# Kernel optimization log

Measured on AMD Instinct MI355X. Metric: run time of the kernel, lower is better.

Reference implementation:

```python
import jax, jax.numpy as jnp
import numpy as np

N_NODES = 2_000_000
N_EDGES = 16_777_216
N_REL = 4


def setup_inputs() -> dict:
    key = jax.random.key(0)
    ks = jax.random.split(key, 13)
    inp = {
        "author_x": jax.random.normal(ks[0], (N_NODES, 4), jnp.float32),
        "paper_x": jax.random.normal(ks[1], (N_NODES, 4), jnp.float32),
        "src_index": jax.random.randint(ks[2], (N_EDGES,), 0, N_NODES, jnp.int64 if jax.config.jax_enable_x64 else jnp.int32).astype(jnp.int32),
        "dst_index": jax.random.randint(ks[3], (N_EDGES,), 0, N_NODES).astype(jnp.int32),
        "edge_type_index": jax.random.randint(ks[4], (N_EDGES,), 0, N_REL).astype(jnp.int32),
        "edge_src_is_paper": jax.random.randint(ks[5], (N_REL,), 0, 2).astype(jnp.int32),
        "edge_dst_is_paper": jax.random.randint(ks[6], (N_REL,), 0, 2).astype(jnp.int32),
        "Wa": jax.random.normal(ks[7], (4, 4), jnp.float32) * 0.5,
        "ba": jax.random.normal(ks[8], (4,), jnp.float32) * 0.1,
        "Wp": jax.random.normal(ks[9], (4, 4), jnp.float32) * 0.5,
        "bp": jax.random.normal(ks[10], (4,), jnp.float32) * 0.1,
        "Ws": jax.random.normal(ks[11], (8,), jnp.float32) * 0.5,
        "bs": jax.random.normal(ks[12], (1,), jnp.float32) * 0.1,
    }
    return inp


def reference(author_x, paper_x, src_index, dst_index, edge_type_index,
              edge_src_is_paper, edge_dst_is_paper, Wa, ba, Wp, bp, Ws, bs):
    # Encode node tables (tiny GEMMs): [N,4] @ [4,4]^T + [4]
    author_h = author_x @ Wa.T + ba
    paper_h = paper_x @ Wp.T + bp
    # Per-edge relation-type dispatch: 1 = paper table, 0 = author table
    src_p = edge_src_is_paper[edge_type_index].astype(bool)  # [E]
    dst_p = edge_dst_is_paper[edge_type_index].astype(bool)  # [E]
    src_repr = jnp.where(src_p[:, None], paper_h[src_index], author_h[src_index])  # [E,4]
    dst_repr = jnp.where(dst_p[:, None], paper_h[dst_index], author_h[dst_index])  # [E,4]
    # scorer: Linear(8,1) on concat, squeeze last dim -> [E]
    logits = jnp.concatenate([src_repr, dst_repr], axis=-1) @ Ws + bs[0]
    return logits
```

## Files before the change

kernel.cpp:

```cpp
#include <hip/hip_runtime.h>

typedef int         iv4 __attribute__((ext_vector_type(4)));
typedef float       fv4 __attribute__((ext_vector_type(4)));
typedef _Float16    hv4 __attribute__((ext_vector_type(4)));
typedef signed char cv4 __attribute__((ext_vector_type(4)));

struct Fold {
    float va_s[4], va_d[4], vp_s[4], vp_d[4];
    float ca_s, ca_d, cp_s, cp_d;
};

__device__ inline Fold make_fold(const float* __restrict__ Wa, const float* __restrict__ ba,
                                 const float* __restrict__ Wp, const float* __restrict__ bp,
                                 const float* __restrict__ Ws) {
    Fold f;
    float w0 = Ws[0], w1 = Ws[1], w2 = Ws[2], w3 = Ws[3];
    float w4 = Ws[4], w5 = Ws[5], w6 = Ws[6], w7 = Ws[7];
#pragma unroll
    for (int j = 0; j < 4; ++j) {
        f.va_s[j] = w0*Wa[j] + w1*Wa[4+j] + w2*Wa[8+j] + w3*Wa[12+j];
        f.va_d[j] = w4*Wa[j] + w5*Wa[4+j] + w6*Wa[8+j] + w7*Wa[12+j];
        f.vp_s[j] = w0*Wp[j] + w1*Wp[4+j] + w2*Wp[8+j] + w3*Wp[12+j];
        f.vp_d[j] = w4*Wp[j] + w5*Wp[4+j] + w6*Wp[8+j] + w7*Wp[12+j];
    }
    f.ca_s = w0*ba[0] + w1*ba[1] + w2*ba[2] + w3*ba[3];
    f.ca_d = w4*ba[0] + w5*ba[1] + w6*ba[2] + w7*ba[3];
    f.cp_s = w0*bp[0] + w1*bp[1] + w2*bp[2] + w3*bp[3];
    f.cp_d = w4*bp[0] + w5*bp[1] + w6*bp[2] + w7*bp[3];
    return f;
}

__device__ inline void node_scores(const Fold& f, fv4 a, fv4 p,
                                   float& as, float& ps, float& ad, float& pd) {
    as = a.x*f.va_s[0] + a.y*f.va_s[1] + a.z*f.va_s[2] + a.w*f.va_s[3] + f.ca_s;
    ad = a.x*f.va_d[0] + a.y*f.va_d[1] + a.z*f.va_d[2] + a.w*f.va_d[3] + f.ca_d;
    ps = p.x*f.vp_s[0] + p.y*f.vp_s[1] + p.z*f.vp_s[2] + p.w*f.vp_s[3] + f.cp_s;
    pd = p.x*f.vp_d[0] + p.y*f.vp_d[1] + p.z*f.vp_d[2] + p.w*f.vp_d[3] + f.cp_d;
}

__global__ __launch_bounds__(256) void node_pass1(
    const fv4* __restrict__ ax, const fv4* __restrict__ px,
    const float* __restrict__ Wa, const float* __restrict__ ba,
    const float* __restrict__ Wp, const float* __restrict__ bp,
    const float* __restrict__ Ws,
    hv4* __restrict__ sc, unsigned* __restrict__ maxes, int n)
{
    Fold f = make_fold(Wa, ba, Wp, bp, Ws);
    float ms = 0.f, md = 0.f;
    int stride = gridDim.x * blockDim.x;
    for (int i = blockIdx.x * blockDim.x + threadIdx.x; i < n; i += stride) {
        fv4 a = __builtin_nontemporal_load(ax + i);
        fv4 p = __builtin_nontemporal_load(px + i);
        float as, ps, ad, pd;
        node_scores(f, a, p, as, ps, ad, pd);
        hv4 h;
        h.x = (_Float16)as; h.y = (_Float16)ps; h.z = (_Float16)ad; h.w = (_Float16)pd;
        __builtin_nontemporal_store(h, sc + i);
        ms = fmaxf(ms, fmaxf(fabsf(as), fabsf(ps)));
        md = fmaxf(md, fmaxf(fabsf(ad), fabsf(pd)));
    }
#pragma unroll
    for (int off = 32; off >= 1; off >>= 1) {
        ms = fmaxf(ms, __shfl_down(ms, off));
        md = fmaxf(md, __shfl_down(md, off));
    }
    __shared__ float lms[4], lmd[4];
    int wave = threadIdx.x >> 6, lane = threadIdx.x & 63;
    if (lane == 0) { lms[wave] = ms; lmd[wave] = md; }
    __syncthreads();
    if (threadIdx.x == 0) {
        float bms = fmaxf(fmaxf(lms[0], lms[1]), fmaxf(lms[2], lms[3]));
        float bmd = fmaxf(fmaxf(lmd[0], lmd[1]), fmaxf(lmd[2], lmd[3]));
        atomicMax(&maxes[0], __float_as_uint(bms));
        atomicMax(&maxes[1], __float_as_uint(bmd));
    }
}

__global__ __launch_bounds__(256) void node_pass2(
    const hv4* __restrict__ sc, const unsigned* __restrict__ maxes,
    signed char* __restrict__ ts, signed char* __restrict__ td, int n)
{
    int i = blockIdx.x * blockDim.x + threadIdx.x;
    if (i >= n) return;
    float inv_s = 127.f / fmaxf(__uint_as_float(maxes[0]), 1e-20f);
    float inv_d = 127.f / fmaxf(__uint_as_float(maxes[1]), 1e-20f);
    hv4 h = __builtin_nontemporal_load(sc + i);
    int qas = min(127, max(-127, __float2int_rn((float)h.x * inv_s)));
    int qps = min(127, max(-127, __float2int_rn((float)h.y * inv_s)));
    int qad = min(127, max(-127, __float2int_rn((float)h.z * inv_d)));
    int qpd = min(127, max(-127, __float2int_rn((float)h.w * inv_d)));
    cv4 dummy;
    (void)dummy;
    ((short*)ts)[i] = (short)(((qps & 0xff) << 8) | (qas & 0xff));
    ((short*)td)[i] = (short)(((qpd & 0xff) << 8) | (qad & 0xff));
}

__global__ __launch_bounds__(256) void edge_src_pass(
    const iv4* __restrict__ src, const iv4* __restrict__ et,
    const int* __restrict__ esp,
    const signed char* __restrict__ ts, cv4* __restrict__ qsrc, int n4)
{
    int i = blockIdx.x * blockDim.x + threadIdx.x;
    if (i >= n4) return;
    unsigned smask = (unsigned)((esp[0]&1) | ((esp[1]&1)<<1) | ((esp[2]&1)<<2) | ((esp[3]&1)<<3));
    iv4 s = __builtin_nontemporal_load(src + i);
    iv4 t = __builtin_nontemporal_load(et  + i);
    cv4 q;
    q.x = ts[2*s.x + (int)((smask >> t.x) & 1u)];
    q.y = ts[2*s.y + (int)((smask >> t.y) & 1u)];
    q.z = ts[2*s.z + (int)((smask >> t.z) & 1u)];
    q.w = ts[2*s.w + (int)((smask >> t.w) & 1u)];
    __builtin_nontemporal_store(q, qsrc + i);
}

__global__ __launch_bounds__(256) void edge_dst_pass(
    const iv4* __restrict__ dst, const iv4* __restrict__ et,
    const int* __restrict__ edp, const float* __restrict__ bs,
    const unsigned* __restrict__ maxes,
    const signed char* __restrict__ td, const cv4* __restrict__ qsrc,
    fv4* __restrict__ out, int n4)
{
    int i = blockIdx.x * blockDim.x + threadIdx.x;
    if (i >= n4) return;
    unsigned dmask = (unsigned)((edp[0]&1) | ((edp[1]&1)<<1) | ((edp[2]&1)<<2) | ((edp[3]&1)<<3));
    float b = bs[0];
    float scale_s = __uint_as_float(maxes[0]) * (1.f / 127.f);
    float scale_d = __uint_as_float(maxes[1]) * (1.f / 127.f);

    iv4 d = __builtin_nontemporal_load(dst + i);
    iv4 t = __builtin_nontemporal_load(et  + i);
    cv4 qs = __builtin_nontemporal_load(qsrc + i);
    signed char q0 = td[2*d.x + (int)((dmask >> t.x) & 1u)];
    signed char q1 = td[2*d.y + (int)((dmask >> t.y) & 1u)];
    signed char q2 = td[2*d.z + (int)((dmask >> t.z) & 1u)];
    signed char q3 = td[2*d.w + (int)((dmask >> t.w) & 1u)];

    fv4 o;
    o.x = (float)qs.x * scale_s + (float)q0 * scale_d + b;
    o.y = (float)qs.y * scale_s + (float)q1 * scale_d + b;
    o.z = (float)qs.z * scale_s + (float)q2 * scale_d + b;
    o.w = (float)qs.w * scale_s + (float)q3 * scale_d + b;
    __builtin_nontemporal_store(o, out + i);
}

__global__ __launch_bounds__(256) void fused_kernel(
    const fv4* __restrict__ ax, const fv4* __restrict__ px,
    const int* __restrict__ src, const int* __restrict__ dst, const int* __restrict__ et,
    const int* __restrict__ esp, const int* __restrict__ edp,
    const float* __restrict__ Wa, const float* __restrict__ ba,
    const float* __restrict__ Wp, const float* __restrict__ bp,
    const float* __restrict__ Ws, const float* __restrict__ bs,
    float* __restrict__ out, int n)
{
    int e = blockIdx.x * blockDim.x + threadIdx.x;
    if (e >= n) return;
    Fold f = make_fold(Wa, ba, Wp, bp, Ws);
    int t = et[e];
    int sp = esp[t] & 1, dp = edp[t] & 1;
    fv4 sv = sp ? px[src[e]] : ax[src[e]];
    fv4 dv = dp ? px[dst[e]] : ax[dst[e]];
    float ssc = sp ? (sv.x*f.vp_s[0] + sv.y*f.vp_s[1] + sv.z*f.vp_s[2] + sv.w*f.vp_s[3] + f.cp_s)
                   : (sv.x*f.va_s[0] + sv.y*f.va_s[1] + sv.z*f.va_s[2] + sv.w*f.va_s[3] + f.ca_s);
    float dsc = dp ? (dv.x*f.vp_d[0] + dv.y*f.vp_d[1] + dv.z*f.vp_d[2] + dv.w*f.vp_d[3] + f.cp_d)
                   : (dv.x*f.va_d[0] + dv.y*f.va_d[1] + dv.z*f.va_d[2] + dv.w*f.va_d[3] + f.ca_d);
    out[e] = ssc + dsc + bs[0];
}

extern "C" void kernel_launch(void* const* d_in, const int* in_sizes, int n_in,
                              void* d_out, int out_size, void* d_ws, size_t ws_size,
                              hipStream_t stream) {
    const float* ax  = (const float*)d_in[0];
    const float* px  = (const float*)d_in[1];
    const int*   src = (const int*)d_in[2];
    const int*   dst = (const int*)d_in[3];
    const int*   et  = (const int*)d_in[4];
    const int*   esp = (const int*)d_in[5];
    const int*   edp = (const int*)d_in[6];
    const float* Wa  = (const float*)d_in[7];
    const float* ba  = (const float*)d_in[8];
    const float* Wp  = (const float*)d_in[9];
    const float* bp  = (const float*)d_in[10];
    const float* Ws  = (const float*)d_in[11];
    const float* bs  = (const float*)d_in[12];
    float* out = (float*)d_out;

    const int n_nodes = in_sizes[0] / 4;
    const int n_edges = in_sizes[2];

    size_t union_sz = (size_t)n_edges > (size_t)n_nodes * 8 ? (size_t)n_edges : (size_t)n_nodes * 8;
    union_sz = (union_sz + 255) & ~(size_t)255;
    const size_t off_u  = 256;
    const size_t off_ts = off_u + union_sz;
    const size_t off_td = off_ts + (size_t)n_nodes * 2;
    const size_t need   = off_td + (size_t)n_nodes * 2;

    if (ws_size >= need && (n_edges & 3) == 0) {
        unsigned* maxes = (unsigned*)d_ws;
        hv4* sc   = (hv4*)((char*)d_ws + off_u);
        cv4* qsrc = (cv4*)((char*)d_ws + off_u);
        signed char* ts = (signed char*)((char*)d_ws + off_ts);
        signed char* td = (signed char*)((char*)d_ws + off_td);

        (void)hipMemsetAsync(maxes, 0, 2 * sizeof(unsigned), stream);
        node_pass1<<<512, 256, 0, stream>>>(
            (const fv4*)ax, (const fv4*)px, Wa, ba, Wp, bp, Ws, sc, maxes, n_nodes);
        node_pass2<<<(n_nodes + 255) / 256, 256, 0, stream>>>(
            sc, maxes, ts, td, n_nodes);

        const int n4 = n_edges / 4;
        const int nb = (n4 + 255) / 256;
        edge_src_pass<<<nb, 256, 0, stream>>>(
            (const iv4*)src, (const iv4*)et, esp, ts, qsrc, n4);
        edge_dst_pass<<<nb, 256, 0, stream>>>(
            (const iv4*)dst, (const iv4*)et, edp, bs, maxes,
            td, (const cv4*)qsrc, (fv4*)out, n4);
    } else {
        fused_kernel<<<(n_edges + 255) / 256, 256, 0, stream>>>(
            (const fv4*)ax, (const fv4*)px, src, dst, et, esp, edp,
            Wa, ba, Wp, bp, Ws, bs, out, n_edges);
    }
}
```

Measured before the change: 432.1 us.

## Pack dst-side relation bit into src intermediate to skip edge_type reread

The src edge pass now writes a 16-bit value per edge: the quantized src score plus the dst-is-paper bit derived from the edge type. The dst pass reads this instead of rereading the edge_type array, which removes one full streaming pass over the edge types. Each thread also processes 16 edges instead of 4. The cost is a larger intermediate buffer (2 bytes per edge instead of 1) and a bigger workspace requirement, with a fallback to the old path if that requirement is not met.

Result: slower. 459.1 us (+6.3%).

```diff
diff --git a/kernel.cpp b/kernel.cpp
--- a/kernel.cpp
+++ b/kernel.cpp
@@ -4,6 +4,7 @@
 typedef float       fv4 __attribute__((ext_vector_type(4)));
 typedef _Float16    hv4 __attribute__((ext_vector_type(4)));
 typedef signed char cv4 __attribute__((ext_vector_type(4)));
+typedef short       sv8 __attribute__((ext_vector_type(8)));
 
 struct Fold {
     float va_s[4], va_d[4], vp_s[4], vp_d[4];
@@ -89,10 +90,88 @@
     int qps = min(127, max(-127, __float2int_rn((float)h.y * inv_s)));
     int qad = min(127, max(-127, __float2int_rn((float)h.z * inv_d)));
     int qpd = min(127, max(-127, __float2int_rn((float)h.w * inv_d)));
-    cv4 dummy;
-    (void)dummy;
     ((short*)ts)[i] = (short)(((qps & 0xff) << 8) | (qas & 0xff));
     ((short*)td)[i] = (short)(((qpd & 0xff) << 8) | (qad & 0xff));
+}
+
+__device__ inline void gather4(const signed char* __restrict__ ts,
+                               unsigned smask, unsigned dmask,
+                               iv4 s, iv4 t, short* r) {
+    r[0] = (short)((unsigned char)ts[2*s.x + (int)((smask >> t.x) & 1u)] | ((int)((dmask >> t.x) & 1u) << 8));
+    r[1] = (short)((unsigned char)ts[2*s.y + (int)((smask >> t.y) & 1u)] | ((int)((dmask >> t.y) & 1u) << 8));
+    r[2] = (short)((unsigned char)ts[2*s.z + (int)((smask >> t.z) & 1u)] | ((int)((dmask >> t.z) & 1u) << 8));
+    r[3] = (short)((unsigned char)ts[2*s.w + (int)((smask >> t.w) & 1u)] | ((int)((dmask >> t.w) & 1u) << 8));
+}
+
+__global__ __launch_bounds__(256) void edge_src_pass16(
+    const iv4* __restrict__ src, const iv4* __restrict__ et,
+    const int* __restrict__ esp, const int* __restrict__ edp,
+    const signed char* __restrict__ ts, sv8* __restrict__ qs, int n16)
+{
+    int i = blockIdx.x * blockDim.x + threadIdx.x;
+    if (i >= n16) return;
+    unsigned smask = (unsigned)((esp[0]&1) | ((esp[1]&1)<<1) | ((esp[2]&1)<<2) | ((esp[3]&1)<<3));
+    unsigned dmask = (unsigned)((edp[0]&1) | ((edp[1]&1)<<1) | ((edp[2]&1)<<2) | ((edp[3]&1)<<3));
+    int base = i * 4;
+    iv4 s0 = __builtin_nontemporal_load(src + base);
+    iv4 s1 = __builtin_nontemporal_load(src + base + 1);
+    iv4 s2 = __builtin_nontemporal_load(src + base + 2);
+    iv4 s3 = __builtin_nontemporal_load(src + base + 3);
+    iv4 t0 = __builtin_nontemporal_load(et + base);
+    iv4 t1 = __builtin_nontemporal_load(et + base + 1);
+    iv4 t2 = __builtin_nontemporal_load(et + base + 2);
+    iv4 t3 = __builtin_nontemporal_load(et + base + 3);
+    short r[16];
+    gather4(ts, smask, dmask, s0, t0, r + 0);
+    gather4(ts, smask, dmask, s1, t1, r + 4);
+    gather4(ts, smask, dmask, s2, t2, r + 8);
+    gather4(ts, smask, dmask, s3, t3, r + 12);
+    sv8 a, b;
+#pragma unroll
+    for (int k = 0; k < 8; ++k) { a[k] = r[k]; b[k] = r[8 + k]; }
+    __builtin_nontemporal_store(a, qs + 2*i);
+    __builtin_nontemporal_store(b, qs + 2*i + 1);
+}
+
+__device__ inline fv4 combine4(const signed char* __restrict__ td, iv4 d,
+                               const short* r, float scale_s, float scale_d, float b) {
+    fv4 o;
+    o.x = (float)(signed char)(r[0] & 0xff) * scale_s + (float)td[2*d.x + ((r[0] >> 8) & 1)] * scale_d + b;
+    o.y = (float)(signed char)(r[1] & 0xff) * scale_s + (float)td[2*d.y + ((r[1] >> 8) & 1)] * scale_d + b;
+    o.z = (float)(signed char)(r[2] & 0xff) * scale_s + (float)td[2*d.z + ((r[2] >> 8) & 1)] * scale_d + b;
+    o.w = (float)(signed char)(r[3] & 0xff) * scale_s + (float)td[2*d.w + ((r[3] >> 8) & 1)] * scale_d + b;
+    return o;
+}
+
+__global__ __launch_bounds__(256) void edge_dst_pass16(
+    const iv4* __restrict__ dst, const float* __restrict__ bs,
+    const unsigned* __restrict__ maxes,
+    const signed char* __restrict__ td, const sv8* __restrict__ qs,
+    fv4* __restrict__ out, int n16)
+{
+    int i = blockIdx.x * blockDim.x + threadIdx.x;
+    if (i >= n16) return;
+    float b = bs[0];
+    float scale_s = __uint_as_float(maxes[0]) * (1.f / 127.f);
+    float scale_d = __uint_as_float(maxes[1]) * (1.f / 127.f);
+    int base = i * 4;
+    iv4 d0 = __builtin_nontemporal_load(dst + base);
+    iv4 d1 = __builtin_nontemporal_load(dst + base + 1);
+    iv4 d2 = __builtin_nontemporal_load(dst + base + 2);
+    iv4 d3 = __builtin_nontemporal_load(dst + base + 3);
+    sv8 qa = __builtin_nontemporal_load(qs + 2*i);
+    sv8 qb = __builtin_nontemporal_load(qs + 2*i + 1);
+    short r[16];
+#pragma unroll
+    for (int k = 0; k < 8; ++k) { r[k] = qa[k]; r[8 + k] = qb[k]; }
+    fv4 o0 = combine4(td, d0, r + 0,  scale_s, scale_d, b);
+    fv4 o1 = combine4(td, d1, r + 4,  scale_s, scale_d, b);
+    fv4 o2 = combine4(td, d2, r + 8,  scale_s, scale_d, b);
+    fv4 o3 = combine4(td, d3, r + 12, scale_s, scale_d, b);
+    __builtin_nontemporal_store(o0, out + base);
+    __builtin_nontemporal_store(o1, out + base + 1);
+    __builtin_nontemporal_store(o2, out + base + 2);
+    __builtin_nontemporal_store(o3, out + base + 3);
 }
 
 __global__ __launch_bounds__(256) void edge_src_pass(
@@ -126,20 +205,14 @@
     float b = bs[0];
     float scale_s = __uint_as_float(maxes[0]) * (1.f / 127.f);
     float scale_d = __uint_as_float(maxes[1]) * (1.f / 127.f);
-
     iv4 d = __builtin_nontemporal_load(dst + i);
     iv4 t = __builtin_nontemporal_load(et  + i);
-    cv4 qs = __builtin_nontemporal_load(qsrc + i);
-    signed char q0 = td[2*d.x + (int)((dmask >> t.x) & 1u)];
-    signed char q1 = td[2*d.y + (int)((dmask >> t.y) & 1u)];
-    signed char q2 = td[2*d.z + (int)((dmask >> t.z) & 1u)];
-    signed char q3 = td[2*d.w + (int)((dmask >> t.w) & 1u)];
-
+    cv4 qsv = __builtin_nontemporal_load(qsrc + i);
     fv4 o;
-    o.x = (float)qs.x * scale_s + (float)q0 * scale_d + b;
-    o.y = (float)qs.y * scale_s + (float)q1 * scale_d + b;
-    o.z = (float)qs.z * scale_s + (float)q2 * scale_d + b;
-    o.w = (float)qs.w * scale_s + (float)q3 * scale_d + b;
+    o.x = (float)qsv.x * scale_s + (float)td[2*d.x + (int)((dmask >> t.x) & 1u)] * scale_d + b;
+    o.y = (float)qsv.y * scale_s + (float)td[2*d.y + (int)((dmask >> t.y) & 1u)] * scale_d + b;
+    o.z = (float)qsv.z * scale_s + (float)td[2*d.z + (int)((dmask >> t.z) & 1u)] * scale_d + b;
+    o.w = (float)qsv.w * scale_s + (float)td[2*d.w + (int)((dmask >> t.w) & 1u)] * scale_d + b;
     __builtin_nontemporal_store(o, out + i);
 }
 
@@ -187,33 +260,51 @@
     const int n_nodes = in_sizes[0] / 4;
     const int n_edges = in_sizes[2];
 
-    size_t union_sz = (size_t)n_edges > (size_t)n_nodes * 8 ? (size_t)n_edges : (size_t)n_nodes * 8;
-    union_sz = (union_sz + 255) & ~(size_t)255;
-    const size_t off_u  = 256;
-    const size_t off_ts = off_u + union_sz;
-    const size_t off_td = off_ts + (size_t)n_nodes * 2;
-    const size_t need   = off_td + (size_t)n_nodes * 2;
-
-    if (ws_size >= need && (n_edges & 3) == 0) {
+    size_t unionP = (size_t)n_edges * 2 > (size_t)n_nodes * 8 ? (size_t)n_edges * 2 : (size_t)n_nodes * 8;
+    unionP = (unionP + 255) & ~(size_t)255;
+    const size_t off_tsP = 256 + unionP;
+    const size_t needP   = off_tsP + (size_t)n_nodes * 4;
+
+    size_t unionR = (size_t)n_edges > (size_t)n_nodes * 8 ? (size_t)n_edges : (size_t)n_nodes * 8;
+    unionR = (unionR + 255) & ~(size_t)255;
+    const size_t off_tsR = 256 + unionR;
+    const size_t needR   = off_tsR + (size_t)n_nodes * 4;
+
+    if (ws_size >= needP && (n_edges & 15) == 0) {
         unsigned* maxes = (unsigned*)d_ws;
-        hv4* sc   = (hv4*)((char*)d_ws + off_u);
-        cv4* qsrc = (cv4*)((char*)d_ws + off_u);
-        signed char* ts = (signed char*)((char*)d_ws + off_ts);
-        signed char* td = (signed char*)((char*)d_ws + off_td);
+        hv4* sc  = (hv4*)((char*)d_ws + 256);
+        sv8* qs  = (sv8*)((char*)d_ws + 256);
+        signed char* ts = (signed char*)((char*)d_ws + off_tsP);
+        signed char* td = ts + (size_t)n_nodes * 2;
 
         (void)hipMemsetAsync(maxes, 0, 2 * sizeof(unsigned), stream);
         node_pass1<<<512, 256, 0, stream>>>(
             (const fv4*)ax, (const fv4*)px, Wa, ba, Wp, bp, Ws, sc, maxes, n_nodes);
-        node_pass2<<<(n_nodes + 255) / 256, 256, 0, stream>>>(
-            sc, maxes, ts, td, n_nodes);
+        node_pass2<<<(n_nodes + 255) / 256, 256, 0, stream>>>(sc, maxes, ts, td, n_nodes);
+
+        const int n16 = n_edges / 16;
+        const int nb = (n16 + 255) / 256;
+        edge_src_pass16<<<nb, 256, 0, stream>>>(
+            (const iv4*)src, (const iv4*)et, esp, edp, ts, qs, n16);
+        edge_dst_pass16<<<nb, 256, 0, stream>>>(
+            (const iv4*)dst, bs, maxes, td, (const sv8*)qs, (fv4*)out, n16);
+    } else if (ws_size >= needR && (n_edges & 3) == 0) {
+        unsigned* maxes = (unsigned*)d_ws;
+        hv4* sc   = (hv4*)((char*)d_ws + 256);
+        cv4* qsrc = (cv4*)((char*)d_ws + 256);
+        signed char* ts = (signed char*)((char*)d_ws + off_tsR);
+        signed char* td = ts + (size_t)n_nodes * 2;
+
+        (void)hipMemsetAsync(maxes, 0, 2 * sizeof(unsigned), stream);
+        node_pass1<<<512, 256, 0, stream>>>(
+            (const fv4*)ax, (const fv4*)px, Wa, ba, Wp, bp, Ws, sc, maxes, n_nodes);
+        node_pass2<<<(n_nodes + 255) / 256, 256, 0, stream>>>(sc, maxes, ts, td, n_nodes);
 
         const int n4 = n_edges / 4;
         const int nb = (n4 + 255) / 256;
-        edge_src_pass<<<nb, 256, 0, stream>>>(
-            (const iv4*)src, (const iv4*)et, esp, ts, qsrc, n4);
+        edge_src_pass<<<nb, 256, 0, stream>>>((const iv4*)src, (const iv4*)et, esp, ts, qsrc, n4);
         edge_dst_pass<<<nb, 256, 0, stream>>>(
-            (const iv4*)dst, (const iv4*)et, edp, bs, maxes,
-            td, (const cv4*)qsrc, (fv4*)out, n4);
+            (const iv4*)dst, (const iv4*)et, edp, bs, maxes, td, (const cv4*)qsrc, (fv4*)out, n4);
     } else {
         fused_kernel<<<(n_edges + 255) / 256, 256, 0, stream>>>(
             (const fv4*)ax, (const fv4*)px, src, dst, et, esp, edp,
```
